# Performance work log

Measured on AMD Instinct MI355X. Metric: run time of the kernel, lower is better.

Reference implementation:

```python
import jax, jax.numpy as jnp
import numpy as np

C = 256
HEADS = 8
HEAD_DIM = C // HEADS
SCALE = HEAD_DIM ** -0.5
POOL = 2
LN_EPS = 1e-5


def setup_inputs() -> dict:
    key = jax.random.key(0)
    ks = jax.random.split(key, 10)
    B, H, W = 8, 64, 64
    std = 0.02
    return {
        "x": jax.random.normal(ks[0], (B, C, H, W), jnp.float32),
        "Wq": jax.random.normal(ks[1], (HEADS, C), jnp.float32) * std,
        "Wk": jax.random.normal(ks[2], (HEADS, C), jnp.float32) * std,
        "Wv": jax.random.normal(ks[3], (C, C), jnp.float32) * std,
        "Wsr": jax.random.normal(ks[4], (C, C), jnp.float32) * (2.0 / C) ** 0.5,
        "bsr": jnp.zeros((C,), jnp.float32),
        "gamma": jnp.ones((C,), jnp.float32),
        "beta": jnp.zeros((C,), jnp.float32),
        "Wp": jax.random.normal(ks[5], (C, C), jnp.float32) * std,
        "bp": jnp.zeros((C,), jnp.float32),
    }


def reference(x, Wq, Wk, Wv, Wsr, bsr, gamma, beta, Wp, bp):
    B, Cc, H, W = x.shape
    N = H * W
    # tokens [B, N, C]
    tok = x.reshape(B, Cc, N).transpose(0, 2, 1)
    # q: Linear(C -> heads), per-head scalar query  [B, heads, N]
    q = jnp.einsum("bnc,hc->bhn", tok, Wq)
    # spatial reduction: avgpool(pool_ratio) then 1x1 conv
    xp = x.reshape(B, Cc, H // POOL, POOL, W // POOL, POOL).mean(axis=(3, 5))
    xs = jnp.einsum("bchw,oc->bohw", xp, Wsr) + bsr[None, :, None, None]
    M = (H // POOL) * (W // POOL)
    x_ = xs.reshape(B, Cc, M).transpose(0, 2, 1)  # [B, M, C]
    # LayerNorm + GELU (exact erf, torch default)
    mu = x_.mean(-1, keepdims=True)
    var = ((x_ - mu) ** 2).mean(-1, keepdims=True)
    x_ = (x_ - mu) * jax.lax.rsqrt(var + LN_EPS) * gamma + beta
    x_ = jax.nn.gelu(x_, approximate=False)
    # k: per-head scalar key [B, heads, M]; v: [B, heads, M, head_dim]
    k = jnp.einsum("bmc,hc->bhm", x_, Wk)
    v = jnp.einsum("bmc,oc->bmo", x_, Wv).reshape(B, M, HEADS, HEAD_DIM).transpose(0, 2, 1, 3)
    # rank-1 attention scores [B, heads, N, M]
    attn = jax.nn.softmax(q[:, :, :, None] * k[:, :, None, :] * SCALE, axis=-1)
    out = jnp.einsum("bhnm,bhmd->bhnd", attn, v)  # [B, heads, N, head_dim]
    out = out.transpose(0, 2, 1, 3).reshape(B, N, Cc)
    out = out @ Wp.T + bp
    return out.transpose(0, 2, 1).reshape(B, Cc, H, W)
```

## Files before the change

### kernel.cpp

```cpp
#include <hip/hip_runtime.h>
#include <math.h>


#define NH 8
#define NJ 8
#define NT (NH * NJ)
#define SCALE 0.17677669529663687f

__device__ __constant__ float INVFACT[NJ] = {
    1.0f, 1.0f, 0.5f, 1.6666666666666666e-01f, 4.1666666666666664e-02f,
    8.3333333333333332e-03f, 1.3888888888888889e-03f, 1.9841269841269841e-04f};

__global__ void k0_q_prep(const float* __restrict__ x, const float* __restrict__ Wq,
                          const float* __restrict__ Wsr, const float* __restrict__ Wv,
                          float* __restrict__ q01, float* __restrict__ WsrT,
                          float* __restrict__ WvT) {
    __shared__ float wq[NH * 128];
    const int tid = threadIdx.x;
    const int blk = blockIdx.x;
    if (blk < 256) {
        const int b = blk >> 5, half = (blk >> 4) & 1, nt = blk & 15;
#pragma unroll
        for (int r = 0; r < 4; ++r) {
            int idx = r * 256 + tid;
            int h = idx >> 7, cc = idx & 127;
            wq[idx] = Wq[h * 256 + half * 128 + cc];
        }
        __syncthreads();
        const int n = nt * 256 + tid;
        const float* xb = x + (((size_t)b << 8) + half * 128) * 4096 + n;
        float acc[NH] = {};
#pragma unroll 8
        for (int c = 0; c < 128; ++c) {
            float xv = xb[(size_t)c << 12];
#pragma unroll
            for (int h = 0; h < NH; ++h) acc[h] += xv * wq[h * 128 + c];
        }
#pragma unroll
        for (int h = 0; h < NH; ++h)
            q01[((size_t)(half * 64 + b * 8 + h) << 12) + n] = acc[h];
    } else {
        const float* W = (blk < 288) ? Wsr : Wv;
        float* WT = (blk < 288) ? WsrT : WvT;
        const int c0 = (blk & 31) * 8;
#pragma unroll
        for (int r = 0; r < 2; ++r) {
            int fidx = r * 256 + tid;
            int c = c0 + (fidx >> 6), o4 = (fidx & 63) * 4;
            float4 t;
            t.x = W[(size_t)(o4 + 0) * 256 + c];
            t.y = W[(size_t)(o4 + 1) * 256 + c];
            t.z = W[(size_t)(o4 + 2) * 256 + c];
            t.w = W[(size_t)(o4 + 3) * 256 + c];
            *(float4*)&WT[(size_t)c * 256 + o4] = t;
        }
    }
}

__global__ __launch_bounds__(256, 2) void ka_mega(
        const float* __restrict__ x, const float* __restrict__ WsrT,
        const float* __restrict__ bsr, const float* __restrict__ WvT,
        const float* __restrict__ gamma, const float* __restrict__ beta,
        const float* __restrict__ Wk,
        float* __restrict__ Mpart, float* __restrict__ Spart) {
    __shared__ float smem[11584];
    float* a_pool = smem;
    float* g_lds  = smem + 640;
    float* g_t    = smem + 4800;
    float4* wkv   = (float4*)(smem + 8896);
    float4* glv   = (float4*)(smem + 10944);
    float4* blv   = (float4*)(smem + 11200);
    float* klds   = smem + 11456;

    const int tid = threadIdx.x;
    const int blk = blockIdx.x;
    const int b = blk >> 6, t16 = blk & 63;
    const int pr = t16 >> 1, half = t16 & 1;

    const int ccs = tid >> 3, jg = tid & 7;
    const int mg = tid & 3, og = tid >> 2;

    wkv[tid] = ((const float4*)Wk)[tid];
    wkv[256 + tid] = ((const float4*)Wk)[256 + tid];
    if (tid < 64) {
        glv[tid] = ((const float4*)gamma)[tid];
        blv[tid] = ((const float4*)beta)[tid];
    }

    const size_t xoff = (size_t)pr * 128 + half * 32 + jg * 4;

    float acc[4][4] = {};
    for (int c0 = 0; c0 < 256; c0 += 32) {
        __syncthreads();
        {
            const float* p = x + ((size_t)(b * 256 + c0 + ccs) << 12) + xoff;
            float4 r0 = *(const float4*)p;
            float4 r1 = *(const float4*)(p + 64);
            float2 pv;
            pv.x = 0.25f * ((r0.x + r0.y) + (r1.x + r1.y));
            pv.y = 0.25f * ((r0.z + r0.w) + (r1.z + r1.w));
            *(float2*)&a_pool[ccs * 20 + jg * 2] = pv;
        }
        __syncthreads();
        const float* wsrc = WsrT + ((size_t)c0 << 8) + og * 4;
#pragma unroll
        for (int cc = 0; cc < 32; ++cc) {
            float4 av = *(const float4*)&a_pool[cc * 20 + mg * 4];
            float4 bv = *(const float4*)&wsrc[(size_t)cc << 8];
            float am[4] = {av.x, av.y, av.z, av.w};
            float bo[4] = {bv.x, bv.y, bv.z, bv.w};
#pragma unroll
            for (int i = 0; i < 4; ++i)
#pragma unroll
                for (int j = 0; j < 4; ++j) acc[i][j] += am[i] * bo[j];
        }
    }
    {
        float4 bs = *(const float4*)&bsr[og * 4];
#pragma unroll
        for (int i = 0; i < 4; ++i) {
            float4 w0;
            w0.x = acc[i][0] + bs.x; w0.y = acc[i][1] + bs.y;
            w0.z = acc[i][2] + bs.z; w0.w = acc[i][3] + bs.w;
            *(float4*)&g_lds[(mg * 4 + i) * 260 + og * 4] = w0;
        }
    }
    __syncthreads();

    const int wave = tid >> 6, lane = tid & 63;
    {
        const float4 g4 = glv[lane], be4 = blv[lane];
        float4 wkreg[NH];
#pragma unroll
        for (int h = 0; h < NH; ++h) wkreg[h] = wkv[h * 64 + lane];
        const int cbh = ((wave ^ (lane & 3)) << 2);
        const int r0 = lane << 6;
        float4 gg4[4];
#pragma unroll
        for (int ti = 0; ti < 4; ++ti) {
            const int mm = wave * 4 + ti;
            float4 vv = *(const float4*)&g_lds[mm * 260 + lane * 4];
            float ssum = (vv.x + vv.y) + (vv.z + vv.w);
            float s2 = (vv.x * vv.x + vv.y * vv.y) + (vv.z * vv.z + vv.w * vv.w);
#pragma unroll
            for (int off = 1; off < 64; off <<= 1) {
                ssum += __shfl_xor(ssum, off);
                s2 += __shfl_xor(s2, off);
            }
            const float mu = ssum * (1.f / 256.f);
            const float rstd = rsqrtf(s2 * (1.f / 256.f) - mu * mu + 1e-5f);
            float4 gg;
            {
                float xh;
                xh = (vv.x - mu) * rstd * g4.x + be4.x;
                gg.x = 0.5f * xh * (1.f + erff(xh * 0.70710678118654752f));
                xh = (vv.y - mu) * rstd * g4.y + be4.y;
                gg.y = 0.5f * xh * (1.f + erff(xh * 0.70710678118654752f));
                xh = (vv.z - mu) * rstd * g4.z + be4.z;
                gg.z = 0.5f * xh * (1.f + erff(xh * 0.70710678118654752f));
                xh = (vv.w - mu) * rstd * g4.w + be4.w;
                gg.w = 0.5f * xh * (1.f + erff(xh * 0.70710678118654752f));
            }
            gg4[ti] = gg;
            float acck[NH];
#pragma unroll
            for (int h = 0; h < NH; ++h) {
                float4 w = wkreg[h];
                acck[h] = (gg.x * w.x + gg.y * w.y) + (gg.z * w.z + gg.w * w.w);
            }
#pragma unroll
            for (int off = 1; off < 64; off <<= 1)
#pragma unroll
                for (int h = 0; h < NH; ++h) acck[h] += __shfl_xor(acck[h], off);
            if (lane == 0) {
#pragma unroll
                for (int h = 0; h < NH; ++h) klds[h * 16 + mm] = acck[h];
            }
        }
        float4 t;
#define GT_WRITE(K, COMP)                                                   \
        t.x = gg4[0].COMP; t.y = gg4[1].COMP;                               \
        t.z = gg4[2].COMP; t.w = gg4[3].COMP;                               \
        *(float4*)&g_t[r0 + ((K) << 4) + cbh] = t;
        GT_WRITE(0, x) GT_WRITE(1, y) GT_WRITE(2, z) GT_WRITE(3, w)
#undef GT_WRITE
    }
    __syncthreads();

    float accv[4][4] = {};
    {
        const float* vsrc = WvT + og * 4;
        for (int c0 = 0; c0 < 256; c0 += 32) {
#pragma unroll
            for (int cc = 0; cc < 32; ++cc) {
                const int c = c0 + cc;
                const int swzc = ((c >> 2) & 3) << 2;
                float4 av = *(const float4*)&g_t[(c << 4) + ((mg << 2) ^ swzc)];
                float4 bv = *(const float4*)&vsrc[(size_t)c << 8];
                float am[4] = {av.x, av.y, av.z, av.w};
                float bo[4] = {bv.x, bv.y, bv.z, bv.w};
#pragma unroll
                for (int i = 0; i < 4; ++i)
#pragma unroll
                    for (int j = 0; j < 4; ++j) accv[i][j] += am[i] * bo[j];
            }
        }
    }

    {
        const int h = og >> 3;
        float km[4], pw[4];
#pragma unroll
        for (int i = 0; i < 4; ++i) {
            km[i] = klds[h * 16 + mg * 4 + i];
            pw[i] = 1.f;
        }
        float sacc[NJ];
        float* Mrow = Mpart + ((size_t)blk << 11) + og * 4;
#pragma unroll
        for (int j = 0; j < NJ; ++j) {
            float mo[4];
#pragma unroll
            for (int o = 0; o < 4; ++o)
                mo[o] = (pw[0] * accv[0][o] + pw[1] * accv[1][o]) +
                        (pw[2] * accv[2][o] + pw[3] * accv[3][o]);
            float sj = (pw[0] + pw[1]) + (pw[2] + pw[3]);
#pragma unroll
            for (int i = 0; i < 4; ++i) pw[i] *= km[i];
#pragma unroll
            for (int off = 1; off < 4; off <<= 1) {
#pragma unroll
                for (int o = 0; o < 4; ++o) mo[o] += __shfl_xor(mo[o], off);
                sj += __shfl_xor(sj, off);
            }
            sacc[j] = sj;
            if (mg == 0) {
                float4 w0;
                w0.x = mo[0]; w0.y = mo[1]; w0.z = mo[2]; w0.w = mo[3];
                *(float4*)&Mrow[j * 256] = w0;
            }
        }
        if (mg == 0 && (og & 7) == 0) {
            float* Srow = Spart + ((size_t)blk << 6) + h * 8;
            float4 s0, s1;
            s0.x = sacc[0]; s0.y = sacc[1]; s0.z = sacc[2]; s0.w = sacc[3];
            s1.x = sacc[4]; s1.y = sacc[5]; s1.z = sacc[6]; s1.w = sacc[7];
            *(float4*)&Srow[0] = s0;
            *(float4*)&Srow[4] = s1;
        }
    }
}

__global__ void kc_fold(const float* __restrict__ Mpart,
                        const float* __restrict__ Spart,
                        const float* __restrict__ Wp,
                        float* __restrict__ P, float* __restrict__ S2) {
    const int bh = blockIdx.x;
    const int h = bh & 7, b = bh >> 3;
    const int tid = threadIdx.x;
    __shared__ float Ms[NJ][33];
    {
        const int j = tid >> 5, d = tid & 31;
        const float* src = Mpart + (((size_t)(b * 64) * 8 + j) << 8) + h * 32 + d;
        float s = 0.f;
#pragma unroll 8
        for (int mtn = 0; mtn < 64; ++mtn) s += src[(size_t)mtn << 11];
        Ms[j][d] = s * INVFACT[j];
    }
    if (tid < NJ) {
        const float* src = Spart + ((size_t)(b * 64) << 6) + h * 8 + tid;
        float ss = 0.f;
#pragma unroll 8
        for (int mtn = 0; mtn < 64; ++mtn) ss += src[mtn << 6];
        S2[bh * NJ + tid] = ss * INVFACT[tid];
    }
    __syncthreads();
    const int c = tid;
    float wp[32];
    const float* wrow = Wp + c * 256 + h * 32;
#pragma unroll
    for (int i = 0; i < 8; ++i) {
        float4 t = *(const float4*)(wrow + i * 4);
        wp[i * 4 + 0] = t.x; wp[i * 4 + 1] = t.y;
        wp[i * 4 + 2] = t.z; wp[i * 4 + 3] = t.w;
    }
#pragma unroll
    for (int j = 0; j < NJ; ++j) {
        float s = 0.f;
#pragma unroll
        for (int dd = 0; dd < 32; ++dd) s += wp[dd] * Ms[j][dd];
        P[((size_t)bh * NJ + j) * 256 + c] = s;
    }
}

__global__ void kd_out(const float* __restrict__ q01, const float* __restrict__ S2,
                       const float* __restrict__ P, const float* __restrict__ bp,
                       float* __restrict__ out) {
    __shared__ float p_lds[NT * 264];
    __shared__ float coef_lds[NT * 32];
    __shared__ float s2l[NT];
    const int tid = threadIdx.x;
    const int b = blockIdx.x >> 7, nt = blockIdx.x & 127;
    const int n0 = nt * 32;
    if (tid < NT) s2l[tid] = S2[b * NT + tid];
    const float* Pb = P + (size_t)b * (NT * 256);
#pragma unroll
    for (int r = 0; r < 16; ++r) {
        int fidx = r * 256 + tid;
        int t = fidx >> 6, c4 = (fidx & 63) * 4;
        *(float4*)&p_lds[t * 264 + c4] = *(const float4*)&Pb[t * 256 + c4];
    }
    __syncthreads();
    {
        const int n = tid & 31, h = tid >> 5;
        size_t qi = ((size_t)(b * NH + h) << 12) + n0 + n;
        float a = (q01[qi] + q01[qi + ((size_t)64 << 12)]) * SCALE;
        float den = s2l[h * NJ + NJ - 1];
#pragma unroll
        for (int j = NJ - 2; j >= 0; --j) den = den * a + s2l[h * NJ + j];
        float p = 1.0f / den;
#pragma unroll
        for (int j = 0; j < NJ; ++j) {
            coef_lds[(h * NJ + j) * 32 + n] = p;
            p *= a;
        }
    }
    __syncthreads();
    const int ng = tid & 7, og = tid >> 3;
    float acc[8][4] = {};
#pragma unroll 8
    for (int t = 0; t < NT; ++t) {
        float4 nv = *(const float4*)&coef_lds[t * 32 + ng * 4];
        float4 cv0 = *(const float4*)&p_lds[t * 264 + og * 8];
        float4 cv1 = *(const float4*)&p_lds[t * 264 + og * 8 + 4];
        float nm[4] = {nv.x, nv.y, nv.z, nv.w};
        float cm[8] = {cv0.x, cv0.y, cv0.z, cv0.w, cv1.x, cv1.y, cv1.z, cv1.w};
#pragma unroll
        for (int i = 0; i < 8; ++i)
#pragma unroll
            for (int j = 0; j < 4; ++j) acc[i][j] += cm[i] * nm[j];
    }
    float* ob = out + ((size_t)(b << 8) + og * 8) * 4096 + n0 + ng * 4;
#pragma unroll
    for (int i = 0; i < 8; ++i) {
        float bpc = bp[og * 8 + i];
        float4 r;
        r.x = acc[i][0] + bpc; r.y = acc[i][1] + bpc;
        r.z = acc[i][2] + bpc; r.w = acc[i][3] + bpc;
        *(float4*)(ob + (size_t)i * 4096) = r;
    }
}

extern "C" void kernel_launch(void* const* d_in, const int* in_sizes, int n_in,
                              void* d_out, int out_size, void* d_ws, size_t ws_size,
                              hipStream_t stream) {
    const float* x     = (const float*)d_in[0];
    const float* Wq    = (const float*)d_in[1];
    const float* Wk    = (const float*)d_in[2];
    const float* Wv    = (const float*)d_in[3];
    const float* Wsr   = (const float*)d_in[4];
    const float* bsr   = (const float*)d_in[5];
    const float* gamma = (const float*)d_in[6];
    const float* beta  = (const float*)d_in[7];
    const float* Wp    = (const float*)d_in[8];
    const float* bp    = (const float*)d_in[9];
    float* out = (float*)d_out;

    float* ws    = (float*)d_ws;
    float* Mpart = ws;
    float* Spart = Mpart + 1048576;
    float* q01   = Spart + 32768;
    float* P     = q01 + 524288;
    float* S2    = P + 131072;
    float* WsrT  = S2 + 512;
    float* WvT   = WsrT + 65536;

    k0_q_prep<<<320, 256, 0, stream>>>(x, Wq, Wsr, Wv, q01, WsrT, WvT);
    ka_mega<<<512, 256, 0, stream>>>(x, WsrT, bsr, WvT, gamma, beta, Wk,
                                     Mpart, Spart);
    kc_fold<<<64, 256, 0, stream>>>(Mpart, Spart, Wp, P, S2);
    kd_out<<<1024, 256, 0, stream>>>(q01, S2, P, bp, out);
}
```

Before: 186.0 us.

## Fuse four kernels into one persistent kernel with global atomic barriers

Merges the prep, projection/norm, fold and output kernels into a single 512-block persistent kernel separated by software grid barriers built from atomics and spin-waits. The goal is to remove the launch gaps and drain/fill tails between the four dependent launches. In exchange it adds a memset launch, atomic spin barriers that rely on all 512 blocks being co-resident, and a larger shared-memory footprint that could reduce occupancy. The output phase now loops twice per block instead of running 1024 blocks.

Measured after the change: 335.6 us. +80.4%, slower.

```diff
diff --git a/kernel.cpp b/kernel.cpp
--- a/kernel.cpp
+++ b/kernel.cpp
@@ -6,348 +6,365 @@
 #define NJ 8
 #define NT (NH * NJ)
 #define SCALE 0.17677669529663687f
+#define NBLK 512
 
 __device__ __constant__ float INVFACT[NJ] = {
     1.0f, 1.0f, 0.5f, 1.6666666666666666e-01f, 4.1666666666666664e-02f,
     8.3333333333333332e-03f, 1.3888888888888889e-03f, 1.9841269841269841e-04f};
 
-__global__ void k0_q_prep(const float* __restrict__ x, const float* __restrict__ Wq,
-                          const float* __restrict__ Wsr, const float* __restrict__ Wv,
-                          float* __restrict__ q01, float* __restrict__ WsrT,
-                          float* __restrict__ WvT) {
-    __shared__ float wq[NH * 128];
+__device__ __forceinline__ void gbar(unsigned* cnt, unsigned* flag) {
+    __syncthreads();
+    if (threadIdx.x == 0) {
+        __threadfence();
+        unsigned old = __hip_atomic_fetch_add(cnt, 1u, __ATOMIC_ACQ_REL,
+                                              __HIP_MEMORY_SCOPE_AGENT);
+        if (old == NBLK - 1u) {
+            __hip_atomic_store(flag, 1u, __ATOMIC_RELEASE,
+                               __HIP_MEMORY_SCOPE_AGENT);
+        } else {
+            while (__hip_atomic_load(flag, __ATOMIC_RELAXED,
+                                     __HIP_MEMORY_SCOPE_AGENT) == 0u)
+                __builtin_amdgcn_s_sleep(2);
+        }
+        __threadfence();
+    }
+    __syncthreads();
+}
+
+__global__ __launch_bounds__(256, 2) void mega(
+        const float* __restrict__ x, const float* __restrict__ Wq,
+        const float* __restrict__ Wk, const float* __restrict__ Wv,
+        const float* __restrict__ Wsr, const float* __restrict__ bsr,
+        const float* __restrict__ gamma, const float* __restrict__ beta,
+        const float* __restrict__ Wp, const float* __restrict__ bp,
+        float* __restrict__ out,
+        float* __restrict__ q01, float* __restrict__ WsrT,
+        float* __restrict__ WvT, float* __restrict__ Mpart,
+        float* __restrict__ Spart, float* __restrict__ P,
+        float* __restrict__ S2, unsigned* __restrict__ bar) {
+    __shared__ float smem[19008];
     const int tid = threadIdx.x;
     const int blk = blockIdx.x;
-    if (blk < 256) {
-        const int b = blk >> 5, half = (blk >> 4) & 1, nt = blk & 15;
-#pragma unroll
-        for (int r = 0; r < 4; ++r) {
-            int idx = r * 256 + tid;
-            int h = idx >> 7, cc = idx & 127;
-            wq[idx] = Wq[h * 256 + half * 128 + cc];
-        }
-        __syncthreads();
-        const int n = nt * 256 + tid;
-        const float* xb = x + (((size_t)b << 8) + half * 128) * 4096 + n;
-        float acc[NH] = {};
+
+    if (blk < 320) {
+        float* wq = smem;
+        if (blk < 256) {
+            const int b = blk >> 5, half = (blk >> 4) & 1, nt = blk & 15;
+#pragma unroll
+            for (int r = 0; r < 4; ++r) {
+                int idx = r * 256 + tid;
+                int h = idx >> 7, cc = idx & 127;
+                wq[idx] = Wq[h * 256 + half * 128 + cc];
+            }
+            __syncthreads();
+            const int n = nt * 256 + tid;
+            const float* xb = x + (((size_t)b << 8) + half * 128) * 4096 + n;
+            float acc[NH] = {};
 #pragma unroll 8
-        for (int c = 0; c < 128; ++c) {
-            float xv = xb[(size_t)c << 12];
-#pragma unroll
-            for (int h = 0; h < NH; ++h) acc[h] += xv * wq[h * 128 + c];
-        }
-#pragma unroll
-        for (int h = 0; h < NH; ++h)
-            q01[((size_t)(half * 64 + b * 8 + h) << 12) + n] = acc[h];
-    } else {
-        const float* W = (blk < 288) ? Wsr : Wv;
-        float* WT = (blk < 288) ? WsrT : WvT;
-        const int c0 = (blk & 31) * 8;
-#pragma unroll
-        for (int r = 0; r < 2; ++r) {
-            int fidx = r * 256 + tid;
-            int c = c0 + (fidx >> 6), o4 = (fidx & 63) * 4;
-            float4 t;
-            t.x = W[(size_t)(o4 + 0) * 256 + c];
-            t.y = W[(size_t)(o4 + 1) * 256 + c];
-            t.z = W[(size_t)(o4 + 2) * 256 + c];
-            t.w = W[(size_t)(o4 + 3) * 256 + c];
-            *(float4*)&WT[(size_t)c * 256 + o4] = t;
+            for (int c = 0; c < 128; ++c) {
+                float xv = xb[(size_t)c << 12];
+#pragma unroll
+                for (int h = 0; h < NH; ++h) acc[h] += xv * wq[h * 128 + c];
+            }
+#pragma unroll
+            for (int h = 0; h < NH; ++h)
+                q01[((size_t)(half * 64 + b * 8 + h) << 12) + n] = acc[h];
+        } else {
+            const float* W = (blk < 288) ? Wsr : Wv;
+            float* WT = (blk < 288) ? WsrT : WvT;
+            const int c0 = (blk & 31) * 8;
+#pragma unroll
+            for (int r = 0; r < 2; ++r) {
+                int fidx = r * 256 + tid;
+                int c = c0 + (fidx >> 6), o4 = (fidx & 63) * 4;
+                float4 t;
+                t.x = W[(size_t)(o4 + 0) * 256 + c];
+                t.y = W[(size_t)(o4 + 1) * 256 + c];
+                t.z = W[(size_t)(o4 + 2) * 256 + c];
+                t.w = W[(size_t)(o4 + 3) * 256 + c];
+                *(float4*)&WT[(size_t)c * 256 + o4] = t;
+            }
         }
     }
-}
-
-__global__ __launch_bounds__(256, 2) void ka_mega(
-        const float* __restrict__ x, const float* __restrict__ WsrT,
-        const float* __restrict__ bsr, const float* __restrict__ WvT,
-        const float* __restrict__ gamma, const float* __restrict__ beta,
-        const float* __restrict__ Wk,
-        float* __restrict__ Mpart, float* __restrict__ Spart) {
-    __shared__ float smem[11584];
-    float* a_pool = smem;
-    float* g_lds  = smem + 640;
-    float* g_t    = smem + 4800;
-    float4* wkv   = (float4*)(smem + 8896);
-    float4* glv   = (float4*)(smem + 10944);
-    float4* blv   = (float4*)(smem + 11200);
-    float* klds   = smem + 11456;
-
-    const int tid = threadIdx.x;
-    const int blk = blockIdx.x;
-    const int b = blk >> 6, t16 = blk & 63;
-    const int pr = t16 >> 1, half = t16 & 1;
-
-    const int ccs = tid >> 3, jg = tid & 7;
-    const int mg = tid & 3, og = tid >> 2;
-
-    wkv[tid] = ((const float4*)Wk)[tid];
-    wkv[256 + tid] = ((const float4*)Wk)[256 + tid];
-    if (tid < 64) {
-        glv[tid] = ((const float4*)gamma)[tid];
-        blv[tid] = ((const float4*)beta)[tid];
-    }
-
-    const size_t xoff = (size_t)pr * 128 + half * 32 + jg * 4;
-
-    float acc[4][4] = {};
-    for (int c0 = 0; c0 < 256; c0 += 32) {
-        __syncthreads();
-        {
-            const float* p = x + ((size_t)(b * 256 + c0 + ccs) << 12) + xoff;
-            float4 r0 = *(const float4*)p;
-            float4 r1 = *(const float4*)(p + 64);
-            float2 pv;
-            pv.x = 0.25f * ((r0.x + r0.y) + (r1.x + r1.y));
-            pv.y = 0.25f * ((r0.z + r0.w) + (r1.z + r1.w));
-            *(float2*)&a_pool[ccs * 20 + jg * 2] = pv;
-        }
-        __syncthreads();
-        const float* wsrc = WsrT + ((size_t)c0 << 8) + og * 4;
-#pragma unroll
-        for (int cc = 0; cc < 32; ++cc) {
-            float4 av = *(const float4*)&a_pool[cc * 20 + mg * 4];
-            float4 bv = *(const float4*)&wsrc[(size_t)cc << 8];
-            float am[4] = {av.x, av.y, av.z, av.w};
-            float bo[4] = {bv.x, bv.y, bv.z, bv.w};
-#pragma unroll
-            for (int i = 0; i < 4; ++i)
-#pragma unroll
-                for (int j = 0; j < 4; ++j) acc[i][j] += am[i] * bo[j];
-        }
-    }
+    gbar(bar + 0, bar + 16);
+
     {
-        float4 bs = *(const float4*)&bsr[og * 4];
-#pragma unroll
-        for (int i = 0; i < 4; ++i) {
-            float4 w0;
-            w0.x = acc[i][0] + bs.x; w0.y = acc[i][1] + bs.y;
-            w0.z = acc[i][2] + bs.z; w0.w = acc[i][3] + bs.w;
-            *(float4*)&g_lds[(mg * 4 + i) * 260 + og * 4] = w0;
-        }
-    }
-    __syncthreads();
-
-    const int wave = tid >> 6, lane = tid & 63;
-    {
-        const float4 g4 = glv[lane], be4 = blv[lane];
-        float4 wkreg[NH];
-#pragma unroll
-        for (int h = 0; h < NH; ++h) wkreg[h] = wkv[h * 64 + lane];
-        const int cbh = ((wave ^ (lane & 3)) << 2);
-        const int r0 = lane << 6;
-        float4 gg4[4];
-#pragma unroll
-        for (int ti = 0; ti < 4; ++ti) {
-            const int mm = wave * 4 + ti;
-            float4 vv = *(const float4*)&g_lds[mm * 260 + lane * 4];
-            float ssum = (vv.x + vv.y) + (vv.z + vv.w);
-            float s2 = (vv.x * vv.x + vv.y * vv.y) + (vv.z * vv.z + vv.w * vv.w);
-#pragma unroll
-            for (int off = 1; off < 64; off <<= 1) {
-                ssum += __shfl_xor(ssum, off);
-                s2 += __shfl_xor(s2, off);
-            }
-            const float mu = ssum * (1.f / 256.f);
-            const float rstd = rsqrtf(s2 * (1.f / 256.f) - mu * mu + 1e-5f);
-            float4 gg;
+        float* a_pool = smem;
+        float* g_lds  = smem + 640;
+        float* g_t    = smem + 4800;
+        float4* wkv   = (float4*)(smem + 8896);
+        float4* glv   = (float4*)(smem + 10944);
+        float4* blv   = (float4*)(smem + 11200);
+        float* klds   = smem + 11456;
+
+        const int b = blk >> 6, t16 = blk & 63;
+        const int pr = t16 >> 1, half = t16 & 1;
+        const int ccs = tid >> 3, jg = tid & 7;
+        const int mg = tid & 3, og = tid >> 2;
+
+        wkv[tid] = ((const float4*)Wk)[tid];
+        wkv[256 + tid] = ((const float4*)Wk)[256 + tid];
+        if (tid < 64) {
+            glv[tid] = ((const float4*)gamma)[tid];
+            blv[tid] = ((const float4*)beta)[tid];
+        }
+        const size_t xoff = (size_t)pr * 128 + half * 32 + jg * 4;
+
+        float acc[4][4] = {};
+        for (int c0 = 0; c0 < 256; c0 += 32) {
+            __syncthreads();
             {
-                float xh;
-                xh = (vv.x - mu) * rstd * g4.x + be4.x;
-                gg.x = 0.5f * xh * (1.f + erff(xh * 0.70710678118654752f));
-                xh = (vv.y - mu) * rstd * g4.y + be4.y;
-                gg.y = 0.5f * xh * (1.f + erff(xh * 0.70710678118654752f));
-                xh = (vv.z - mu) * rstd * g4.z + be4.z;
-                gg.z = 0.5f * xh * (1.f + erff(xh * 0.70710678118654752f));
-                xh = (vv.w - mu) * rstd * g4.w + be4.w;
-                gg.w = 0.5f * xh * (1.f + erff(xh * 0.70710678118654752f));
-            }
-            gg4[ti] = gg;
-            float acck[NH];
-#pragma unroll
-            for (int h = 0; h < NH; ++h) {
-                float4 w = wkreg[h];
-                acck[h] = (gg.x * w.x + gg.y * w.y) + (gg.z * w.z + gg.w * w.w);
-            }
-#pragma unroll
-            for (int off = 1; off < 64; off <<= 1)
-#pragma unroll
-                for (int h = 0; h < NH; ++h) acck[h] += __shfl_xor(acck[h], off);
-            if (lane == 0) {
-#pragma unroll
-                for (int h = 0; h < NH; ++h) klds[h * 16 + mm] = acck[h];
-            }
-        }
-        float4 t;
-#define GT_WRITE(K, COMP)                                                   \
-        t.x = gg4[0].COMP; t.y = gg4[1].COMP;                               \
-        t.z = gg4[2].COMP; t.w = gg4[3].COMP;                               \
-        *(float4*)&g_t[r0 + ((K) << 4) + cbh] = t;
-        GT_WRITE(0, x) GT_WRITE(1, y) GT_WRITE(2, z) GT_WRITE(3, w)
-#undef GT_WRITE
-    }
-    __syncthreads();
-
-    float accv[4][4] = {};
-    {
-        const float* vsrc = WvT + og * 4;
-        for (int c0 = 0; c0 < 256; c0 += 32) {
+                const float* p = x + ((size_t)(b * 256 + c0 + ccs) << 12) + xoff;
+                float4 r0 = *(const float4*)p;
+                float4 r1 = *(const float4*)(p + 64);
+                float2 pv;
+                pv.x = 0.25f * ((r0.x + r0.y) + (r1.x + r1.y));
+                pv.y = 0.25f * ((r0.z + r0.w) + (r1.z + r1.w));
+                *(float2*)&a_pool[ccs * 20 + jg * 2] = pv;
+            }
+            __syncthreads();
+            const float* wsrc = WsrT + ((size_t)c0 << 8) + og * 4;
 #pragma unroll
             for (int cc = 0; cc < 32; ++cc) {
-                const int c = c0 + cc;
-                const int swzc = ((c >> 2) & 3) << 2;
-                float4 av = *(const float4*)&g_t[(c << 4) + ((mg << 2) ^ swzc)];
-                float4 bv = *(const float4*)&vsrc[(size_t)c << 8];
+                float4 av = *(const float4*)&a_pool[cc * 20 + mg * 4];
+                float4 bv = *(const float4*)&wsrc[(size_t)cc << 8];
                 float am[4] = {av.x, av.y, av.z, av.w};
                 float bo[4] = {bv.x, bv.y, bv.z, bv.w};
 #pragma unroll
                 for (int i = 0; i < 4; ++i)
 #pragma unroll
-                    for (int j = 0; j < 4; ++j) accv[i][j] += am[i] * bo[j];
+                    for (int j = 0; j < 4; ++j) acc[i][j] += am[i] * bo[j];
+            }
+        }
+        {
+            float4 bs = *(const float4*)&bsr[og * 4];
+#pragma unroll
+            for (int i = 0; i < 4; ++i) {
+                float4 w0;
+                w0.x = acc[i][0] + bs.x; w0.y = acc[i][1] + bs.y;
+                w0.z = acc[i][2] + bs.z; w0.w = acc[i][3] + bs.w;
+                *(float4*)&g_lds[(mg * 4 + i) * 260 + og * 4] = w0;
+            }
+        }
+        __syncthreads();
+
+        const int wave = tid >> 6, lane = tid & 63;
+        {
+            const float4 g4 = glv[lane], be4 = blv[lane];
+            float4 wkreg[NH];
+#pragma unroll
+            for (int h = 0; h < NH; ++h) wkreg[h] = wkv[h * 64 + lane];
+            const int cbh = ((wave ^ (lane & 3)) << 2);
+            const int r0 = lane << 6;
+            float4 gg4[4];
+#pragma unroll
+            for (int ti = 0; ti < 4; ++ti) {
+                const int mm = wave * 4 + ti;
+                float4 vv = *(const float4*)&g_lds[mm * 260 + lane * 4];
+                float ssum = (vv.x + vv.y) + (vv.z + vv.w);
+                float s2 = (vv.x * vv.x + vv.y * vv.y) + (vv.z * vv.z + vv.w * vv.w);
+#pragma unroll
+                for (int off = 1; off < 64; off <<= 1) {
+                    ssum += __shfl_xor(ssum, off);
+                    s2 += __shfl_xor(s2, off);
+                }
+                const float mu = ssum * (1.f / 256.f);
+                const float rstd = rsqrtf(s2 * (1.f / 256.f) - mu * mu + 1e-5f);
+                float4 gg;
+                {
+                    float xh;
+                    xh = (vv.x - mu) * rstd * g4.x + be4.x;
+                    gg.x = 0.5f * xh * (1.f + erff(xh * 0.70710678118654752f));
+                    xh = (vv.y - mu) * rstd * g4.y + be4.y;
+                    gg.y = 0.5f * xh * (1.f + erff(xh * 0.70710678118654752f));
+                    xh = (vv.z - mu) * rstd * g4.z + be4.z;
+                    gg.z = 0.5f * xh * (1.f + erff(xh * 0.70710678118654752f));
+                    xh = (vv.w - mu) * rstd * g4.w + be4.w;
+                    gg.w = 0.5f * xh * (1.f + erff(xh * 0.70710678118654752f));
+                }
+                gg4[ti] = gg;
+                float acck[NH];
+#pragma unroll
+                for (int h = 0; h < NH; ++h) {
+                    float4 w = wkreg[h];
+                    acck[h] = (gg.x * w.x + gg.y * w.y) + (gg.z * w.z + gg.w * w.w);
+                }
+#pragma unroll
+                for (int off = 1; off < 64; off <<= 1)
+#pragma unroll
+                    for (int h = 0; h < NH; ++h) acck[h] += __shfl_xor(acck[h], off);
+                if (lane == 0) {
+#pragma unroll
+                    for (int h = 0; h < NH; ++h) klds[h * 16 + mm] = acck[h];
+                }
+            }
+            float4 t;
+#define GT_WRITE(K, COMP)                                                   \
+            t.x = gg4[0].COMP; t.y = gg4[1].COMP;                           \
+            t.z = gg4[2].COMP; t.w = gg4[3].COMP;                           \
+            *(float4*)&g_t[r0 + ((K) << 4) + cbh] = t;
+            GT_WRITE(0, x) GT_WRITE(1, y) GT_WRITE(2, z) GT_WRITE(3, w)
+#undef GT_WRITE
+        }
+        __syncthreads();
+
+        float accv[4][4] = {};
+        {
+            const float* vsrc = WvT + og * 4;
+            for (int c0 = 0; c0 < 256; c0 += 32) {
+#pragma unroll
+                for (int cc = 0; cc < 32; ++cc) {
+                    const int c = c0 + cc;
+                    const int swzc = ((c >> 2) & 3) << 2;
+                    float4 av = *(const float4*)&g_t[(c << 4) + ((mg << 2) ^ swzc)];
+                    float4 bv = *(const float4*)&vsrc[(size_t)c << 8];
+                    float am[4] = {av.x, av.y, av.z, av.w};
+                    float bo[4] = {bv.x, bv.y, bv.z, bv.w};
+#pragma unroll
+                    for (int i = 0; i < 4; ++i)
+#pragma unroll
+                        for (int j = 0; j < 4; ++j) accv[i][j] += am[i] * bo[j];
+                }
+            }
+        }
+
+        {
+            const int h = og >> 3;
+            float km[4], pw[4];
+#pragma unroll
+            for (int i = 0; i < 4; ++i) {
+                km[i] = klds[h * 16 + mg * 4 + i];
+                pw[i] = 1.f;
+            }
+            float sacc[NJ];
+            float* Mrow = Mpart + ((size_t)blk << 11) + og * 4;
+#pragma unroll
+            for (int j = 0; j < NJ; ++j) {
+                float mo[4];
+#pragma unroll
+                for (int o = 0; o < 4; ++o)
+                    mo[o] = (pw[0] * accv[0][o] + pw[1] * accv[1][o]) +
+                            (pw[2] * accv[2][o] + pw[3] * accv[3][o]);
+                float sj = (pw[0] + pw[1]) + (pw[2] + pw[3]);
+#pragma unroll
+                for (int i = 0; i < 4; ++i) pw[i] *= km[i];
+#pragma unroll
+                for (int off = 1; off < 4; off <<= 1) {
+#pragma unroll
+                    for (int o = 0; o < 4; ++o) mo[o] += __shfl_xor(mo[o], off);
+                    sj += __shfl_xor(sj, off);
+                }
+                sacc[j] = sj;
+                if (mg == 0) {
+                    float4 w0;
+                    w0.x = mo[0]; w0.y = mo[1]; w0.z = mo[2]; w0.w = mo[3];
+                    *(float4*)&Mrow[j * 256] = w0;
+                }
+            }
+            if (mg == 0 && (og & 7) == 0) {
+                float* Srow = Spart + ((size_t)blk << 6) + h * 8;
+                float4 s0, s1;
+                s0.x = sacc[0]; s0.y = sacc[1]; s0.z = sacc[2]; s0.w = sacc[3];
+                s1.x = sacc[4]; s1.y = sacc[5]; s1.z = sacc[6]; s1.w = sacc[7];
+                *(float4*)&Srow[0] = s0;
+                *(float4*)&Srow[4] = s1;
             }
         }
     }
-
-    {
-        const int h = og >> 3;
-        float km[4], pw[4];
-#pragma unroll
-        for (int i = 0; i < 4; ++i) {
-            km[i] = klds[h * 16 + mg * 4 + i];
-            pw[i] = 1.f;
-        }
-        float sacc[NJ];
-        float* Mrow = Mpart + ((size_t)blk << 11) + og * 4;
+    gbar(bar + 32, bar + 48);
+
+    if (blk < 64) {
+        float (*Ms)[33] = (float (*)[33])smem;
+        const int h = blk & 7, b = blk >> 3;
+        {
+            const int j = tid >> 5, d = tid & 31;
+            const float* src = Mpart + (((size_t)(b * 64) * 8 + j) << 8) + h * 32 + d;
+            float s = 0.f;
+#pragma unroll 8
+            for (int mtn = 0; mtn < 64; ++mtn) s += src[(size_t)mtn << 11];
+            Ms[j][d] = s * INVFACT[j];
+        }
+        if (tid < NJ) {
+            const float* src = Spart + ((size_t)(b * 64) << 6) + h * 8 + tid;
+            float ss = 0.f;
+#pragma unroll 8
+            for (int mtn = 0; mtn < 64; ++mtn) ss += src[mtn << 6];
+            S2[blk * NJ + tid] = ss * INVFACT[tid];
+        }
+        __syncthreads();
+        const int c = tid;
+        float wp[32];
+        const float* wrow = Wp + c * 256 + h * 32;
+#pragma unroll
+        for (int i = 0; i < 8; ++i) {
+            float4 t = *(const float4*)(wrow + i * 4);
+            wp[i * 4 + 0] = t.x; wp[i * 4 + 1] = t.y;
+            wp[i * 4 + 2] = t.z; wp[i * 4 + 3] = t.w;
+        }
 #pragma unroll
         for (int j = 0; j < NJ; ++j) {
-            float mo[4];
-#pragma unroll
-            for (int o = 0; o < 4; ++o)
-                mo[o] = (pw[0] * accv[0][o] + pw[1] * accv[1][o]) +
-                        (pw[2] * accv[2][o] + pw[3] * accv[3][o]);
-            float sj = (pw[0] + pw[1]) + (pw[2] + pw[3]);
-#pragma unroll
-            for (int i = 0; i < 4; ++i) pw[i] *= km[i];
-#pragma unroll
-            for (int off = 1; off < 4; off <<= 1) {
-#pragma unroll
-                for (int o = 0; o < 4; ++o) mo[o] += __shfl_xor(mo[o], off);
-                sj += __shfl_xor(sj, off);
-            }
-            sacc[j] = sj;
-            if (mg == 0) {
-                float4 w0;
-                w0.x = mo[0]; w0.y = mo[1]; w0.z = mo[2]; w0.w = mo[3];
-                *(float4*)&Mrow[j * 256] = w0;
-            }
-        }
-        if (mg == 0 && (og & 7) == 0) {
-            float* Srow = Spart + ((size_t)blk << 6) + h * 8;
-            float4 s0, s1;
-            s0.x = sacc[0]; s0.y = sacc[1]; s0.z = sacc[2]; s0.w = sacc[3];
-            s1.x = sacc[4]; s1.y = sacc[5]; s1.z = sacc[6]; s1.w = sacc[7];
-            *(float4*)&Srow[0] = s0;
-            *(float4*)&Srow[4] = s1;
+            float s = 0.f;
+#pragma unroll
+            for (int dd = 0; dd < 32; ++dd) s += wp[dd] * Ms[j][dd];
+            P[((size_t)blk * NJ + j) * 256 + c] = s;
         }
     }
-}
-
-__global__ void kc_fold(const float* __restrict__ Mpart,
-                        const float* __restrict__ Spart,
-                        const float* __restrict__ Wp,
-                        float* __restrict__ P, float* __restrict__ S2) {
-    const int bh = blockIdx.x;
-    const int h = bh & 7, b = bh >> 3;
-    const int tid = threadIdx.x;
-    __shared__ float Ms[NJ][33];
-    {
-        const int j = tid >> 5, d = tid & 31;
-        const float* src = Mpart + (((size_t)(b * 64) * 8 + j) << 8) + h * 32 + d;
-        float s = 0.f;
+    gbar(bar + 64, bar + 80);
+
+    for (int v = blk; v < 1024; v += 512) {
+        float* p_lds    = smem;
+        float* coef_lds = smem + NT * 264;
+        float* s2l      = smem + NT * 264 + NT * 32;
+        const int b = v >> 7, nt = v & 127;
+        const int n0 = nt * 32;
+        __syncthreads();
+        if (tid < NT) s2l[tid] = S2[b * NT + tid];
+        const float* Pb = P + (size_t)b * (NT * 256);
+#pragma unroll
+        for (int r = 0; r < 16; ++r) {
+            int fidx = r * 256 + tid;
+            int t = fidx >> 6, c4 = (fidx & 63) * 4;
+            *(float4*)&p_lds[t * 264 + c4] = *(const float4*)&Pb[t * 256 + c4];
+        }
+        __syncthreads();
+        {
+            const int n = tid & 31, h = tid >> 5;
+            size_t qi = ((size_t)(b * NH + h) << 12) + n0 + n;
+            float a = (q01[qi] + q01[qi + ((size_t)64 << 12)]) * SCALE;
+            float den = s2l[h * NJ + NJ - 1];
+#pragma unroll
+            for (int j = NJ - 2; j >= 0; --j) den = den * a + s2l[h * NJ + j];
+            float p = 1.0f / den;
+#pragma unroll
+            for (int j = 0; j < NJ; ++j) {
+                coef_lds[(h * NJ + j) * 32 + n] = p;
+                p *= a;
+            }
+        }
+        __syncthreads();
+        const int ng = tid & 7, og = tid >> 3;
+        float acc[8][4] = {};
 #pragma unroll 8
-        for (int mtn = 0; mtn < 64; ++mtn) s += src[(size_t)mtn << 11];
-        Ms[j][d] = s * INVFACT[j];
-    }
-    if (tid < NJ) {
-        const float* src = Spart + ((size_t)(b * 64) << 6) + h * 8 + tid;
-        float ss = 0.f;
-#pragma unroll 8
-        for (int mtn = 0; mtn < 64; ++mtn) ss += src[mtn << 6];
-        S2[bh * NJ + tid] = ss * INVFACT[tid];
-    }
-    __syncthreads();
-    const int c = tid;
-    float wp[32];
-    const float* wrow = Wp + c * 256 + h * 32;
-#pragma unroll
-    for (int i = 0; i < 8; ++i) {
-        float4 t = *(const float4*)(wrow + i * 4);
-        wp[i * 4 + 0] = t.x; wp[i * 4 + 1] = t.y;
-        wp[i * 4 + 2] = t.z; wp[i * 4 + 3] = t.w;
-    }
-#pragma unroll
-    for (int j = 0; j < NJ; ++j) {
-        float s = 0.f;
-#pragma unroll
-        for (int dd = 0; dd < 32; ++dd) s += wp[dd] * Ms[j][dd];
-        P[((size_t)bh * NJ + j) * 256 + c] = s;
-    }
-}
-
-__global__ void kd_out(const float* __restrict__ q01, const float* __restrict__ S2,
-                       const float* __restrict__ P, const float* __restrict__ bp,
-                       float* __restrict__ out) {
-    __shared__ float p_lds[NT * 264];
-    __shared__ float coef_lds[NT * 32];
-    __shared__ float s2l[NT];
-    const int tid = threadIdx.x;
-    const int b = blockIdx.x >> 7, nt = blockIdx.x & 127;
-    const int n0 = nt * 32;
-    if (tid < NT) s2l[tid] = S2[b * NT + tid];
-    const float* Pb = P + (size_t)b * (NT * 256);
-#pragma unroll
-    for (int r = 0; r < 16; ++r) {
-        int fidx = r * 256 + tid;
-        int t = fidx >> 6, c4 = (fidx & 63) * 4;
-        *(float4*)&p_lds[t * 264 + c4] = *(const float4*)&Pb[t * 256 + c4];
-    }
-    __syncthreads();
-    {
-        const int n = tid & 31, h = tid >> 5;
-        size_t qi = ((size_t)(b * NH + h) << 12) + n0 + n;
-        float a = (q01[qi] + q01[qi + ((size_t)64 << 12)]) * SCALE;
-        float den = s2l[h * NJ + NJ - 1];
-#pragma unroll
-        for (int j = NJ - 2; j >= 0; --j) den = den * a + s2l[h * NJ + j];
-        float p = 1.0f / den;
-#pragma unroll
-        for (int j = 0; j < NJ; ++j) {
-            coef_lds[(h * NJ + j) * 32 + n] = p;
-            p *= a;
-        }
-    }
-    __syncthreads();
-    const int ng = tid & 7, og = tid >> 3;
-    float acc[8][4] = {};
-#pragma unroll 8
-    for (int t = 0; t < NT; ++t) {
-        float4 nv = *(const float4*)&coef_lds[t * 32 + ng * 4];
-        float4 cv0 = *(const float4*)&p_lds[t * 264 + og * 8];
-        float4 cv1 = *(const float4*)&p_lds[t * 264 + og * 8 + 4];
-        float nm[4] = {nv.x, nv.y, nv.z, nv.w};
-        float cm[8] = {cv0.x, cv0.y, cv0.z, cv0.w, cv1.x, cv1.y, cv1.z, cv1.w};
-#pragma unroll
-        for (int i = 0; i < 8; ++i)
-#pragma unroll
-            for (int j = 0; j < 4; ++j) acc[i][j] += cm[i] * nm[j];
-    }
-    float* ob = out + ((size_t)(b << 8) + og * 8) * 4096 + n0 + ng * 4;
-#pragma unroll
-    for (int i = 0; i < 8; ++i) {
-        float bpc = bp[og * 8 + i];
-        float4 r;
-        r.x = acc[i][0] + bpc; r.y = acc[i][1] + bpc;
-        r.z = acc[i][2] + bpc; r.w = acc[i][3] + bpc;
-        *(float4*)(ob + (size_t)i * 4096) = r;
+        for (int t = 0; t < NT; ++t) {
+            float4 nv = *(const float4*)&coef_lds[t * 32 + ng * 4];
+            float4 cv0 = *(const float4*)&p_lds[t * 264 + og * 8];
+            float4 cv1 = *(const float4*)&p_lds[t * 264 + og * 8 + 4];
+            float nm[4] = {nv.x, nv.y, nv.z, nv.w};
+            float cm[8] = {cv0.x, cv0.y, cv0.z, cv0.w, cv1.x, cv1.y, cv1.z, cv1.w};
+#pragma unroll
+            for (int i = 0; i < 8; ++i)
+#pragma unroll
+                for (int j = 0; j < 4; ++j) acc[i][j] += cm[i] * nm[j];
+        }
+        float* ob = out + ((size_t)(b << 8) + og * 8) * 4096 + n0 + ng * 4;
+#pragma unroll
+        for (int i = 0; i < 8; ++i) {
+            float bpc = bp[og * 8 + i];
+            float4 r;
+            r.x = acc[i][0] + bpc; r.y = acc[i][1] + bpc;
+            r.z = acc[i][2] + bpc; r.w = acc[i][3] + bpc;
+            *(float4*)(ob + (size_t)i * 4096) = r;
+        }
     }
 }
 
@@ -374,10 +391,10 @@
     float* S2    = P + 131072;
     float* WsrT  = S2 + 512;
     float* WvT   = WsrT + 65536;
-
-    k0_q_prep<<<320, 256, 0, stream>>>(x, Wq, Wsr, Wv, q01, WsrT, WvT);
-    ka_mega<<<512, 256, 0, stream>>>(x, WsrT, bsr, WvT, gamma, beta, Wk,
-                                     Mpart, Spart);
-    kc_fold<<<64, 256, 0, stream>>>(Mpart, Spart, Wp, P, S2);
-    kd_out<<<1024, 256, 0, stream>>>(q01, S2, P, bp, out);
+    unsigned* bar = (unsigned*)(WvT + 65536);
+
+    hipMemsetAsync(bar, 0, 96 * sizeof(unsigned), stream);
+    hipLaunchKernelGGL(mega, dim3(512), dim3(256), 0, stream,
+                       x, Wq, Wk, Wv, Wsr, bsr, gamma, beta, Wp, bp,
+                       out, q01, WsrT, WvT, Mpart, Spart, P, S2, bar);
 }
```

## Double-buffer pooled x tiles in ka_mega and read P directly from global in kd_out

Applied to the files above, without the earlier changes.

In ka_mega, the pooled-input staging becomes double-buffered in LDS. The next channel tile's x values are prefetched into registers while the current tile's GEMM runs, which drops one barrier per iteration. In kd_out, the P tile is no longer staged into LDS; each thread reads its P rows straight from global (cache) memory, with launch_bounds raised to allow 4 blocks/SM and the unroll reduced. These changes aim to overlap global loads with compute and to raise occupancy by cutting LDS usage, at the cost of more LDS in ka_mega and repeated global reads of P.

Result: no change. 188.7 us (+1.4%).

```diff
diff --git a/kernel.cpp b/kernel.cpp
--- a/kernel.cpp
+++ b/kernel.cpp
@@ -63,14 +63,14 @@
         const float* __restrict__ gamma, const float* __restrict__ beta,
         const float* __restrict__ Wk,
         float* __restrict__ Mpart, float* __restrict__ Spart) {
-    __shared__ float smem[11584];
+    __shared__ float smem[12224];
     float* a_pool = smem;
-    float* g_lds  = smem + 640;
-    float* g_t    = smem + 4800;
-    float4* wkv   = (float4*)(smem + 8896);
-    float4* glv   = (float4*)(smem + 10944);
-    float4* blv   = (float4*)(smem + 11200);
-    float* klds   = smem + 11456;
+    float* g_lds  = smem + 1280;
+    float* g_t    = smem + 5440;
+    float4* wkv   = (float4*)(smem + 9536);
+    float4* glv   = (float4*)(smem + 11584);
+    float4* blv   = (float4*)(smem + 11840);
+    float* klds   = smem + 12096;
 
     const int tid = threadIdx.x;
     const int blk = blockIdx.x;
@@ -88,24 +88,42 @@
     }
 
     const size_t xoff = (size_t)pr * 128 + half * 32 + jg * 4;
+    const float* xbase = x + (((size_t)b << 8) << 12) + xoff;
 
     float acc[4][4] = {};
-    for (int c0 = 0; c0 < 256; c0 += 32) {
-        __syncthreads();
-        {
-            const float* p = x + ((size_t)(b * 256 + c0 + ccs) << 12) + xoff;
-            float4 r0 = *(const float4*)p;
-            float4 r1 = *(const float4*)(p + 64);
+    float4 xa, xb_;
+    {
+        const float* p = xbase + ((size_t)ccs << 12);
+        float4 r0 = *(const float4*)p;
+        float4 r1 = *(const float4*)(p + 64);
+        float2 pv;
+        pv.x = 0.25f * ((r0.x + r0.y) + (r1.x + r1.y));
+        pv.y = 0.25f * ((r0.z + r0.w) + (r1.z + r1.w));
+        *(float2*)&a_pool[ccs * 20 + jg * 2] = pv;
+    }
+    {
+        const float* p = xbase + ((size_t)(32 + ccs) << 12);
+        xa = *(const float4*)p;
+        xb_ = *(const float4*)(p + 64);
+    }
+    __syncthreads();
+    for (int p = 0; p < 8; ++p) {
+        if (p < 7) {
             float2 pv;
-            pv.x = 0.25f * ((r0.x + r0.y) + (r1.x + r1.y));
-            pv.y = 0.25f * ((r0.z + r0.w) + (r1.z + r1.w));
-            *(float2*)&a_pool[ccs * 20 + jg * 2] = pv;
-        }
-        __syncthreads();
-        const float* wsrc = WsrT + ((size_t)c0 << 8) + og * 4;
+            pv.x = 0.25f * ((xa.x + xa.y) + (xb_.x + xb_.y));
+            pv.y = 0.25f * ((xa.z + xa.w) + (xb_.z + xb_.w));
+            *(float2*)&a_pool[((p + 1) & 1) * 640 + ccs * 20 + jg * 2] = pv;
+        }
+        if (p < 6) {
+            const float* px = xbase + ((size_t)((p + 2) * 32 + ccs) << 12);
+            xa = *(const float4*)px;
+            xb_ = *(const float4*)(px + 64);
+        }
+        const float* ap = a_pool + (p & 1) * 640;
+        const float* wsrc = WsrT + ((size_t)(p * 32) << 8) + og * 4;
 #pragma unroll
         for (int cc = 0; cc < 32; ++cc) {
-            float4 av = *(const float4*)&a_pool[cc * 20 + mg * 4];
+            float4 av = *(const float4*)&ap[cc * 20 + mg * 4];
             float4 bv = *(const float4*)&wsrc[(size_t)cc << 8];
             float am[4] = {av.x, av.y, av.z, av.w};
             float bo[4] = {bv.x, bv.y, bv.z, bv.w};
@@ -114,6 +132,7 @@
 #pragma unroll
                 for (int j = 0; j < 4; ++j) acc[i][j] += am[i] * bo[j];
         }
+        __syncthreads();
     }
     {
         float4 bs = *(const float4*)&bsr[og * 4];
@@ -293,23 +312,16 @@
     }
 }
 
-__global__ void kd_out(const float* __restrict__ q01, const float* __restrict__ S2,
-                       const float* __restrict__ P, const float* __restrict__ bp,
-                       float* __restrict__ out) {
-    __shared__ float p_lds[NT * 264];
+__global__ __launch_bounds__(256, 4) void kd_out(
+        const float* __restrict__ q01, const float* __restrict__ S2,
+        const float* __restrict__ P, const float* __restrict__ bp,
+        float* __restrict__ out) {
     __shared__ float coef_lds[NT * 32];
     __shared__ float s2l[NT];
     const int tid = threadIdx.x;
     const int b = blockIdx.x >> 7, nt = blockIdx.x & 127;
     const int n0 = nt * 32;
     if (tid < NT) s2l[tid] = S2[b * NT + tid];
-    const float* Pb = P + (size_t)b * (NT * 256);
-#pragma unroll
-    for (int r = 0; r < 16; ++r) {
-        int fidx = r * 256 + tid;
-        int t = fidx >> 6, c4 = (fidx & 63) * 4;
-        *(float4*)&p_lds[t * 264 + c4] = *(const float4*)&Pb[t * 256 + c4];
-    }
     __syncthreads();
     {
         const int n = tid & 31, h = tid >> 5;
@@ -327,12 +339,13 @@
     }
     __syncthreads();
     const int ng = tid & 7, og = tid >> 3;
+    const float* Pb = P + (size_t)b * (NT * 256) + og * 8;
     float acc[8][4] = {};
-#pragma unroll 8
+#pragma unroll 4
     for (int t = 0; t < NT; ++t) {
         float4 nv = *(const float4*)&coef_lds[t * 32 + ng * 4];
-        float4 cv0 = *(const float4*)&p_lds[t * 264 + og * 8];
-        float4 cv1 = *(const float4*)&p_lds[t * 264 + og * 8 + 4];
+        float4 cv0 = *(const float4*)&Pb[t * 256];
+        float4 cv1 = *(const float4*)&Pb[t * 256 + 4];
         float nm[4] = {nv.x, nv.y, nv.z, nv.w};
         float cm[8] = {cv0.x, cv0.y, cv0.z, cv0.w, cv1.x, cv1.y, cv1.z, cv1.w};
 #pragma unroll
```
